# Kernel optimization log

Measured on AMD Instinct MI355X. Metric: run time of the kernel, lower is better.

Reference implementation:

```python
import jax, jax.numpy as jnp
import numpy as np

G, S = 4, 2
EPS_GN, EPS_COS = 1e-5, 1e-8


def group_norm(x, w, b, groups):
    B, C, H, W = x.shape
    xg = x.reshape(B, groups, C // groups, H, W)
    m = xg.mean(axis=(2, 3, 4), keepdims=True)
    v = ((xg - m) ** 2).mean(axis=(2, 3, 4), keepdims=True)
    xn = ((xg - m) / jnp.sqrt(v + EPS_GN)).reshape(B, C, H, W)
    return xn * w[None, :, None, None] + b[None, :, None, None]


def compute_similarity(x, k=3, dilation=2):
    # cosine similarity (over channels) between each pixel and its 8 dilated
    # neighbors (zero padded, unfold row-major order, center dropped)
    B, C, H, W = x.shape
    pad = (k // 2) * dilation
    xp = jnp.pad(x, ((0, 0), (0, 0), (pad, pad), (pad, pad)))
    cn = jnp.sqrt(jnp.sum(x * x, axis=1))  # (B,H,W)
    sims = []
    for ki in range(k):
        for kj in range(k):
            if ki == k // 2 and kj == k // 2:
                continue
            nb = jax.lax.dynamic_slice(xp, (0, 0, ki * dilation, kj * dilation), (B, C, H, W))
            dot = jnp.sum(x * nb, axis=1)
            nn_ = jnp.sqrt(jnp.sum(nb * nb, axis=1))
            sims.append(dot / jnp.maximum(cn * nn_, EPS_COS))
    return jnp.stack(sims, axis=1)  # (B, k*k-1, H, W)


def conv1x1_bn(x, w, sc, bi):
    # 1x1 conv (no bias) followed by eval-mode BN folded to per-channel scale/shift
    return jnp.einsum('oc,bchw->bohw', w, x) * sc[None, :, None, None] + bi[None, :, None, None]


def pixel_unshuffle(x, r):
    B, C, H, W = x.shape
    return x.reshape(B, C, H // r, r, W // r, r).transpose(0, 1, 3, 5, 2, 4).reshape(B, C * r * r, H // r, W // r)


def pixel_shuffle(x, r):
    B, C, H, W = x.shape
    return x.reshape(B, C // (r * r), r, r, H, W).transpose(0, 1, 4, 2, 5, 3).reshape(B, C // (r * r), H * r, W * r)


def init_pos(dtype):
    h = jnp.arange((-S + 1) / 2, (S - 1) / 2 + 1, dtype=dtype) / S  # [-0.25, 0.25]
    t = jnp.stack(jnp.meshgrid(h, h, indexing='ij')).transpose(0, 2, 1)  # (2,2,2)
    return jnp.tile(t, (1, G, 1)).reshape(1, -1, 1, 1)  # (1, 2*g*s*s, 1, 1)


def grid_sample_border(x, grid):
    # bilinear, align_corners=False, padding_mode='border'
    N, C, H, W = x.shape
    gx = jnp.clip(((grid[..., 0] + 1) * W - 1) / 2, 0.0, W - 1.0)
    gy = jnp.clip(((grid[..., 1] + 1) * H - 1) / 2, 0.0, H - 1.0)
    x0 = jnp.floor(gx)
    y0 = jnp.floor(gy)
    wx = (gx - x0)[..., None]
    wy = (gy - y0)[..., None]
    x0i = x0.astype(jnp.int32)
    y0i = y0.astype(jnp.int32)
    x1i = jnp.minimum(x0i + 1, W - 1)
    y1i = jnp.minimum(y0i + 1, H - 1)
    bi = jnp.arange(N)[:, None, None]
    v00 = x[bi, :, y0i, x0i]  # (N,Ho,Wo,C)
    v01 = x[bi, :, y0i, x1i]
    v10 = x[bi, :, y1i, x0i]
    v11 = x[bi, :, y1i, x1i]
    out = (v00 * (1 - wx) + v01 * wx) * (1 - wy) + (v10 * (1 - wx) + v11 * wx) * wy
    return out.transpose(0, 3, 1, 2)  # (N,C,Ho,Wo)


def sample(x, offset):
    b, _, h, w = offset.shape
    off = offset.reshape(b, 2, -1, h, w)  # (b,2,g*s*s,h,w)
    cw = jnp.arange(w, dtype=x.dtype) + 0.5
    ch = jnp.arange(h, dtype=x.dtype) + 0.5
    coords = jnp.stack(jnp.meshgrid(cw, ch, indexing='ij')).transpose(0, 2, 1)[None, :, None]  # (1,2,1,h,w)
    norm = jnp.array([w, h], dtype=x.dtype).reshape(1, 2, 1, 1, 1)
    coords = 2 * (coords + off) / norm - 1
    grid = pixel_shuffle(coords.reshape(b, -1, h, w), S)  # (b, 2*g, s*h, s*w)
    grid = grid.reshape(b, 2, G, S * h, S * w).transpose(0, 2, 3, 4, 1).reshape(b * G, S * h, S * w, 2)
    C = x.shape[1]
    out = grid_sample_border(x.reshape(b * G, C // G, h, w), grid)
    return out.reshape(b, C, S * h, S * w)


def setup_inputs() -> dict:
    key = jax.random.key(0)
    ks = jax.random.split(key, 24)
    B, C, H, W, CF = 2, 64, 128, 128, 256
    CIN, C2L, C2H = C + 8, 2 * G * S * S, 2 * G
    f = jnp.float32
    return {
        'x_l': jax.random.normal(ks[0], (B, C, H, W), f),
        'x_h': jax.random.normal(ks[1], (B, C, 2 * H, 2 * W), f),
        'feat2sample': jax.random.normal(ks[2], (B, CF, H, W), f),
        'gn_l_w': 1.0 + 0.1 * jax.random.normal(ks[3], (C,), f),
        'gn_l_b': 0.1 * jax.random.normal(ks[4], (C,), f),
        'gn_h_w': 1.0 + 0.1 * jax.random.normal(ks[5], (C,), f),
        'gn_h_b': 0.1 * jax.random.normal(ks[6], (C,), f),
        'w_off': 0.02 * jax.random.normal(ks[7], (C2L, CIN), f),
        's_off': 1.0 + 0.05 * jax.random.normal(ks[8], (C2L,), f),
        'b_off': 0.02 * jax.random.normal(ks[9], (C2L,), f),
        'w_off_h': 0.02 * jax.random.normal(ks[10], (C2H, CIN), f),
        's_off_h': 1.0 + 0.05 * jax.random.normal(ks[11], (C2H,), f),
        'b_off_h': 0.02 * jax.random.normal(ks[12], (C2H,), f),
        'w_ds': 0.02 * jax.random.normal(ks[13], (C2L, CIN), f),
        's_ds': 1.0 + 0.05 * jax.random.normal(ks[14], (C2L,), f),
        'b_ds': 0.02 * jax.random.normal(ks[15], (C2L,), f),
        'w_ds_h': 0.02 * jax.random.normal(ks[16], (C2H, CIN), f),
        's_ds_h': 1.0 + 0.05 * jax.random.normal(ks[17], (C2H,), f),
        'b_ds_h': 0.02 * jax.random.normal(ks[18], (C2H,), f),
    }


def reference(x_l, x_h, feat2sample, gn_l_w, gn_l_b, gn_h_w, gn_h_b,
              w_off, s_off, b_off, w_off_h, s_off_h, b_off_h,
              w_ds, s_ds, b_ds, w_ds_h, s_ds_h, b_ds_h):
    xl = group_norm(x_l, gn_l_w, gn_l_b, x_l.shape[1] // 8)
    xh = group_norm(x_h, gn_h_w, gn_h_b, x_h.shape[1] // 8)
    sim_l = jnp.concatenate([xl, compute_similarity(xl)], axis=1)  # (B, C+8, H, W)
    sim_h = jnp.concatenate([xh, compute_similarity(xh)], axis=1)  # (B, C+8, 2H, 2W)
    off = conv1x1_bn(sim_l, w_off, s_off, b_off) \
        + pixel_unshuffle(conv1x1_bn(sim_h, w_off_h, s_off_h, b_off_h), S)
    gate = jax.nn.sigmoid(conv1x1_bn(sim_l, w_ds, s_ds, b_ds)
                          + pixel_unshuffle(conv1x1_bn(sim_h, w_ds_h, s_ds_h, b_ds_h), S))
    offset = off * gate + init_pos(xl.dtype)  # (B, 2*g*s*s, H, W)
    return sample(feat2sample, offset)
```

## Files before the change

### kernel.cpp

```cpp
#include <hip/hip_runtime.h>
#include <math.h>

#define BATCH 2
#define CCH 64
#define HL 128
#define WL 128
#define HH 256
#define WH 256
#define CFCH 256
#define CIN 72

constexpr long WS_AL   = 0;
constexpr long WS_BL   = 128;
constexpr long WS_AH   = 256;
constexpr long WS_BH   = 384;
constexpr long WS_OFFL = 512;
constexpr long WS_DSL  = WS_OFFL + 1048576;
constexpr long WS_OFFH = WS_DSL + 1048576;
constexpr long WS_DSH  = WS_OFFH + 1048576;
constexpr long WS_CRD  = WS_DSH + 1048576;
constexpr long WS_PART = WS_CRD + 1048576;

__global__ void k_stats1(const float* __restrict__ xl, const float* __restrict__ xh,
                         float* __restrict__ ws) {
  int blk = blockIdx.x;
  const float* x;
  long base;
  int gg, slice;
  if (blk < 256) {
    int g = blk >> 4; slice = blk & 15;
    x = xl; gg = g;
    base = (long)g * 8 * (HL * WL) + (long)slice * 8192;
  } else {
    int id = blk - 256;
    int g = id >> 6; slice = id & 63;
    x = xh; gg = 16 + g;
    base = (long)g * 8 * (HH * WH) + (long)slice * 8192;
  }
  const float4* p = (const float4*)(x + base);
  float s = 0.f, s2 = 0.f;
  #pragma unroll
  for (int k = 0; k < 8; k++) {
    float4 v = p[threadIdx.x + k * 256];
    s  += v.x + v.y + v.z + v.w;
    s2 += v.x * v.x + v.y * v.y + v.z * v.z + v.w * v.w;
  }
  __shared__ float sh1[256], sh2[256];
  sh1[threadIdx.x] = s; sh2[threadIdx.x] = s2;
  __syncthreads();
  for (int off = 128; off > 0; off >>= 1) {
    if (threadIdx.x < off) {
      sh1[threadIdx.x] += sh1[threadIdx.x + off];
      sh2[threadIdx.x] += sh2[threadIdx.x + off];
    }
    __syncthreads();
  }
  if (threadIdx.x == 0) {
    ws[WS_PART + (gg * 64 + slice) * 2]     = sh1[0];
    ws[WS_PART + (gg * 64 + slice) * 2 + 1] = sh2[0];
  }
}

__global__ void k_stats2(const float* __restrict__ gwl, const float* __restrict__ gbl,
                         const float* __restrict__ gwh, const float* __restrict__ gbh,
                         float* __restrict__ ws) {
  int blk = blockIdx.x;
  bool high = blk >= 16;
  int id = blk & 15;
  int b = id >> 3, g = id & 7;
  int gg = high ? 16 + id : id;
  int nsl = high ? 64 : 16;
  long n = high ? (long)8 * HH * WH : (long)8 * HL * WL;
  float s = 0.f, s2 = 0.f;
  for (int i = threadIdx.x; i < nsl; i += 64) {
    s  += ws[WS_PART + (gg * 64 + i) * 2];
    s2 += ws[WS_PART + (gg * 64 + i) * 2 + 1];
  }
  for (int off = 32; off > 0; off >>= 1) {
    s  += __shfl_down(s, off);
    s2 += __shfl_down(s2, off);
  }
  __shared__ float shm[2];
  if (threadIdx.x == 0) { shm[0] = s; shm[1] = s2; }
  __syncthreads();
  if (threadIdx.x < 8) {
    float mean = shm[0] / (float)n;
    float var  = shm[1] / (float)n - mean * mean;
    float inv  = rsqrtf(var + 1e-5f);
    int c = g * 8 + threadIdx.x;
    const float* gw = high ? gwh : gwl;
    const float* gb = high ? gbh : gbl;
    float a  = gw[c] * inv;
    float bb = gb[c] - mean * a;
    float* abase = ws + (high ? WS_AH : WS_AL);
    abase[b * CCH + c] = a;
    abase[128 + b * CCH + c] = bb;
  }
}

template<int HSZ, int WSZ, int NOUT>
__global__ __launch_bounds__(512) void k_head(
                       const float* __restrict__ x,
                       const float* __restrict__ w_off, const float* __restrict__ w_ds,
                       const float* __restrict__ s_off, const float* __restrict__ b_off,
                       const float* __restrict__ s_ds,  const float* __restrict__ b_ds,
                       const float* __restrict__ acoef, const float* __restrict__ bcoef,
                       float* __restrict__ out_off, float* __restrict__ out_ds) {
  constexpr int HW   = HSZ * WSZ;
  constexpr int half = NOUT / 2;
  constexpr int PER  = NOUT / 8;
  __shared__ float wsm[NOUT * CIN];
  __shared__ float xc[CCH * 64];
  __shared__ float psum[8 * 64];
  __shared__ float sims[8 * 64];
  __shared__ float asm_[CCH], bsm_[CCH];

  int tid = threadIdx.x;
  int px = tid & 63;
  int t  = tid >> 6;
  int gpix = blockIdx.x * 64 + px;
  int xq = gpix % WSZ;
  int yq = (gpix / WSZ) % HSZ;
  int bq = gpix / (WSZ * HSZ);

  for (int i = tid; i < NOUT * CIN; i += 512) {
    int o = i / CIN, c = i % CIN;
    wsm[i] = (o < half) ? w_off[o * CIN + c] : w_ds[(o - half) * CIN + c];
  }
  if (tid < CCH)            asm_[tid] = acoef[bq * CCH + tid];
  else if (tid < 2 * CCH)   bsm_[tid - CCH] = bcoef[bq * CCH + tid - CCH];
  __syncthreads();

  const float* ptr = x + ((long)(bq * CCH)) * HW + yq * WSZ + xq;

  {
    float ss = 0.f;
    #pragma unroll
    for (int k = 0; k < 8; k++) {
      int c = t * 8 + k;
      float v = fmaf(asm_[c], ptr[(long)c * HW], bsm_[c]);
      xc[c * 64 + px] = v;
      ss += v * v;
    }
    psum[t * 64 + px] = ss;
  }
  __syncthreads();

  {
    const int dyv[8] = {-2,-2,-2, 0, 0, 2, 2, 2};
    const int dxv[8] = {-2, 0, 2,-2, 2,-2, 0, 2};
    int dy = dyv[t], dx = dxv[t];
    int yn = yq + dy;
    int xn = xq + dx;
    bool ok = (yn >= 0 && yn < HSZ && xn >= 0 && xn < WSZ);
    float dot = 0.f, nbq = 0.f;
    if (ok) {
      const float* nptr = ptr + (long)dy * WSZ + dx;
      #pragma unroll 16
      for (int c = 0; c < CCH; c++) {
        float nb = fmaf(asm_[c], nptr[(long)c * HW], bsm_[c]);
        float xv = xc[c * 64 + px];
        dot += xv * nb;
        nbq += nb * nb;
      }
    }
    float cs = 0.f;
    #pragma unroll
    for (int tt = 0; tt < 8; tt++) cs += psum[tt * 64 + px];
    float cnc = sqrtf(cs);
    sims[t * 64 + px] = dot / fmaxf(cnc * sqrtf(nbq), 1e-8f);
  }
  __syncthreads();

  {
    float sv[8];
    #pragma unroll
    for (int j = 0; j < 8; j++) sv[j] = sims[j * 64 + px];
    float acc[PER];
    #pragma unroll
    for (int ol = 0; ol < PER; ol++) acc[ol] = 0.f;
    int o0 = t * PER;
    #pragma unroll 4
    for (int c = 0; c < CCH; c += 4) {
      float x0v = xc[(c + 0) * 64 + px];
      float x1v = xc[(c + 1) * 64 + px];
      float x2v = xc[(c + 2) * 64 + px];
      float x3v = xc[(c + 3) * 64 + px];
      #pragma unroll
      for (int ol = 0; ol < PER; ol++) {
        const float4 w4 = *(const float4*)&wsm[(o0 + ol) * CIN + c];
        acc[ol] += w4.x * x0v + w4.y * x1v + w4.z * x2v + w4.w * x3v;
      }
    }
    #pragma unroll
    for (int ol = 0; ol < PER; ol++) {
      const float4 wa = *(const float4*)&wsm[(o0 + ol) * CIN + 64];
      const float4 wb = *(const float4*)&wsm[(o0 + ol) * CIN + 68];
      acc[ol] += wa.x * sv[0] + wa.y * sv[1] + wa.z * sv[2] + wa.w * sv[3]
               + wb.x * sv[4] + wb.y * sv[5] + wb.z * sv[6] + wb.w * sv[7];
    }
    #pragma unroll
    for (int ol = 0; ol < PER; ol++) {
      int o = o0 + ol;
      float v;
      float* dst;
      int oo;
      if (o < half) { v = acc[ol] * s_off[o] + b_off[o];             dst = out_off; oo = o; }
      else          { v = acc[ol] * s_ds[o - half] + b_ds[o - half]; dst = out_ds;  oo = o - half; }
      dst[((long)(bq * half + oo)) * HW + yq * WSZ + xq] = v;
    }
  }
}

__global__ __launch_bounds__(256) void k_combine(float* __restrict__ ws) {
  int idx = blockIdx.x * blockDim.x + threadIdx.x;
  int x = idx & 127;
  int y = (idx >> 7) & 127;
  int sub = (idx >> 14) & 15;
  int b = idx >> 18;
  int sdx = sub & 1, sdy = (sub >> 1) & 1;

  const float* offl = ws + WS_OFFL;
  const float* dsl  = ws + WS_DSL;
  const float* offh = ws + WS_OFFH;
  const float* dsh  = ws + WS_DSH;

  int lidx = idx + b * (16 * HL * WL);
  float ol0 = offl[lidx],               dl0 = dsl[lidx];
  float ol1 = offl[lidx + 16 * HL * WL], dl1 = dsl[lidx + 16 * HL * WL];
  int Y = 2 * y + sdy, X = 2 * x + sdx;
  long h0 = ((long)(b * 8 + (sub >> 2)) * HH + Y) * WH + X;
  long h1 = h0 + (long)4 * HH * WH;
  float oh0 = offh[h0], dh0 = dsh[h0];
  float oh1 = offh[h1], dh1 = dsh[h1];
  float gate0 = 1.f / (1.f + expf(-(dl0 + dh0)));
  float gate1 = 1.f / (1.f + expf(-(dl1 + dh1)));
  float offx = (ol0 + oh0) * gate0 + (sdx ? 0.25f : -0.25f);
  float offy = (ol1 + oh1) * gate1 + (sdy ? 0.25f : -0.25f);
  float gx = fminf(fmaxf((float)x + offx, 0.f), (float)(WL - 1));
  float gy = fminf(fmaxf((float)y + offy, 0.f), (float)(HL - 1));
  float2* crd = (float2*)(ws + WS_CRD);
  crd[idx] = float2{gx, gy};
}

__global__ __launch_bounds__(512, 6) void k_sample(const float* __restrict__ feat,
                                                   const float* __restrict__ ws,
                                                   float* __restrict__ out) {
  __shared__ float sbuf[8 * 512];
  int bid = (blockIdx.x & 7) * 128 + (blockIdx.x >> 3);
  int y = bid & 127;
  int g = (bid >> 7) & 3;
  int b = bid >> 9;
  int w = threadIdx.x >> 6;
  int l = threadIdx.x & 63;

  const float2* crd = (const float2*)(ws + WS_CRD);
  int   pack[8];
  float wxa[8], wya[8];
  bool fb = false;
  #pragma unroll
  for (int Yp = 0; Yp < 2; Yp++) {
    #pragma unroll
    for (int j = 0; j < 4; j++) {
      int xx = 2 * l + (j >> 1);
      int sub = 4 * g + 2 * Yp + (j & 1);
      float2 cc = crd[((long)(b * 16 + sub)) * (HL * WL) + y * WL + xx];
      float gx = cc.x, gy = cc.y;
      float fx0 = floorf(gx), fy0 = floorf(gy);
      int x0 = (int)fx0, y0 = (int)fy0;
      float wx = gx - fx0, wy = gy - fy0;
      if (x0 >= WL - 1) { x0 = WL - 2; wx = 1.f; }
      if (y0 >= HL - 1) { y0 = HL - 2; wy = 1.f; }
      fb = fb || (y0 < y - 1) || (y0 > y + 1);
      pack[Yp * 4 + j] = y0 * WL + x0;
      wxa[Yp * 4 + j] = wx;
      wya[Yp * 4 + j] = wy;
    }
  }
  int ladj = w * 512 + (1 - y) * 128;

  int row0 = l >> 5;
  int row1 = 2 + row0;
  int fr0 = min(max(y - 1 + row0, 0), HL - 1);
  int fr1 = min(max(y - 1 + row1, 0), HL - 1);
  int x4 = (l & 31) * 4;
  long cbase = (long)(b * CFCH + g * 64 + w);
  const float* ps0 = feat + (cbase * HL + fr0) * WL + x4;
  const float* ps1 = feat + (cbase * HL + fr1) * WL + x4;
  const float* pg  = feat + cbase * (HL * WL);
  int s0 = w * 512 + row0 * 128 + x4;
  int s1 = w * 512 + row1 * 128 + x4;
  float* po0 = out + (cbase * HH + 2 * y) * WH + 4 * l;
  float* po1 = po0 + WH;
  const long CSTEP  = (long)8 * HL * WL;
  const long OSTEP  = (long)8 * HH * WH;

  float4 t0 = *(const float4*)ps0;
  float4 t1 = *(const float4*)ps1;
  #pragma unroll 1
  for (int k = 0; k < 8; k++) {
    *(float4*)&sbuf[s0] = t0;
    *(float4*)&sbuf[s1] = t1;
    if (k < 7) {
      ps0 += CSTEP; ps1 += CSTEP;
      t0 = *(const float4*)ps0;
      t1 = *(const float4*)ps1;
    }
    float v[2][4];
    if (!fb) {
      #pragma unroll
      for (int Yp = 0; Yp < 2; Yp++) {
        #pragma unroll
        for (int j = 0; j < 4; j++) {
          int li = pack[Yp * 4 + j] + ladj;
          float wx = wxa[Yp * 4 + j], wy = wya[Yp * 4 + j];
          float s00 = sbuf[li], s01 = sbuf[li + 1];
          float s10 = sbuf[li + 128], s11 = sbuf[li + 129];
          v[Yp][j] = (s00 * (1.f - wx) + s01 * wx) * (1.f - wy)
                   + (s10 * (1.f - wx) + s11 * wx) * wy;
        }
      }
    } else {
      #pragma unroll
      for (int Yp = 0; Yp < 2; Yp++) {
        #pragma unroll
        for (int j = 0; j < 4; j++) {
          const float* pp = pg + pack[Yp * 4 + j];
          float wx = wxa[Yp * 4 + j], wy = wya[Yp * 4 + j];
          float s00 = pp[0], s01 = pp[1];
          float s10 = pp[WL], s11 = pp[WL + 1];
          v[Yp][j] = (s00 * (1.f - wx) + s01 * wx) * (1.f - wy)
                   + (s10 * (1.f - wx) + s11 * wx) * wy;
        }
      }
    }
    *(float4*)po0 = make_float4(v[0][0], v[0][1], v[0][2], v[0][3]);
    *(float4*)po1 = make_float4(v[1][0], v[1][1], v[1][2], v[1][3]);
    po0 += OSTEP; po1 += OSTEP;
    pg  += CSTEP;
  }
}

extern "C" void kernel_launch(void* const* d_in, const int* in_sizes, int n_in,
                              void* d_out, int out_size, void* d_ws, size_t ws_size,
                              hipStream_t stream) {
  const float* x_l     = (const float*)d_in[0];
  const float* x_h     = (const float*)d_in[1];
  const float* feat    = (const float*)d_in[2];
  const float* gn_l_w  = (const float*)d_in[3];
  const float* gn_l_b  = (const float*)d_in[4];
  const float* gn_h_w  = (const float*)d_in[5];
  const float* gn_h_b  = (const float*)d_in[6];
  const float* w_off   = (const float*)d_in[7];
  const float* s_off   = (const float*)d_in[8];
  const float* b_off   = (const float*)d_in[9];
  const float* w_off_h = (const float*)d_in[10];
  const float* s_off_h = (const float*)d_in[11];
  const float* b_off_h = (const float*)d_in[12];
  const float* w_ds    = (const float*)d_in[13];
  const float* s_ds    = (const float*)d_in[14];
  const float* b_ds    = (const float*)d_in[15];
  const float* w_ds_h  = (const float*)d_in[16];
  const float* s_ds_h  = (const float*)d_in[17];
  const float* b_ds_h  = (const float*)d_in[18];
  float* ws  = (float*)d_ws;
  float* out = (float*)d_out;

  k_stats1<<<1280, 256, 0, stream>>>(x_l, x_h, ws);
  k_stats2<<<32, 64, 0, stream>>>(gn_l_w, gn_l_b, gn_h_w, gn_h_b, ws);
  k_head<HL, WL, 64><<<(BATCH * HL * WL) / 64, 512, 0, stream>>>(
      x_l, w_off, w_ds, s_off, b_off, s_ds, b_ds,
      ws + WS_AL, ws + WS_BL, ws + WS_OFFL, ws + WS_DSL);
  k_head<HH, WH, 16><<<(BATCH * HH * WH) / 64, 512, 0, stream>>>(
      x_h, w_off_h, w_ds_h, s_off_h, b_off_h, s_ds_h, b_ds_h,
      ws + WS_AH, ws + WS_BH, ws + WS_OFFH, ws + WS_DSH);
  k_combine<<<(BATCH * 16 * HL * WL) / 256, 256, 0, stream>>>(ws);
  k_sample<<<BATCH * 4 * HL, 512, 0, stream>>>(feat, ws, out);
}
```

Measured before the change: 99.25 us.

## Split sampling blocks to one output row each, doubling grid size

```diff
diff --git a/kernel.cpp b/kernel.cpp
--- a/kernel.cpp
+++ b/kernel.cpp
@@ -243,39 +243,38 @@
   crd[idx] = float2{gx, gy};
 }
 
-__global__ __launch_bounds__(512, 6) void k_sample(const float* __restrict__ feat,
+__global__ __launch_bounds__(512, 8) void k_sample(const float* __restrict__ feat,
                                                    const float* __restrict__ ws,
                                                    float* __restrict__ out) {
   __shared__ float sbuf[8 * 512];
-  int bid = (blockIdx.x & 7) * 128 + (blockIdx.x >> 3);
-  int y = bid & 127;
-  int g = (bid >> 7) & 3;
-  int b = bid >> 9;
+  int bid = (blockIdx.x & 7) * 256 + (blockIdx.x >> 3);
+  int Y = bid & 255;
+  int g = (bid >> 8) & 3;
+  int b = bid >> 10;
+  int y = Y >> 1, sdy = Y & 1;
   int w = threadIdx.x >> 6;
   int l = threadIdx.x & 63;
 
   const float2* crd = (const float2*)(ws + WS_CRD);
-  int   pack[8];
-  float wxa[8], wya[8];
+  int   pack[4];
+  float wxa[4], wya[4];
   bool fb = false;
   #pragma unroll
-  for (int Yp = 0; Yp < 2; Yp++) {
-    #pragma unroll
-    for (int j = 0; j < 4; j++) {
-      int xx = 2 * l + (j >> 1);
-      int sub = 4 * g + 2 * Yp + (j & 1);
-      float2 cc = crd[((long)(b * 16 + sub)) * (HL * WL) + y * WL + xx];
-      float gx = cc.x, gy = cc.y;
-      float fx0 = floorf(gx), fy0 = floorf(gy);
-      int x0 = (int)fx0, y0 = (int)fy0;
-      float wx = gx - fx0, wy = gy - fy0;
-      if (x0 >= WL - 1) { x0 = WL - 2; wx = 1.f; }
-      if (y0 >= HL - 1) { y0 = HL - 2; wy = 1.f; }
-      fb = fb || (y0 < y - 1) || (y0 > y + 1);
-      pack[Yp * 4 + j] = y0 * WL + x0;
-      wxa[Yp * 4 + j] = wx;
-      wya[Yp * 4 + j] = wy;
-    }
+  for (int j = 0; j < 4; j++) {
+    int X = 4 * l + j;
+    int x = X >> 1, sdx = X & 1;
+    int sub = 4 * g + 2 * sdy + sdx;
+    float2 cc = crd[((long)(b * 16 + sub)) * (HL * WL) + y * WL + x];
+    float gx = cc.x, gy = cc.y;
+    float fx0 = floorf(gx), fy0 = floorf(gy);
+    int x0 = (int)fx0, y0 = (int)fy0;
+    float wx = gx - fx0, wy = gy - fy0;
+    if (x0 >= WL - 1) { x0 = WL - 2; wx = 1.f; }
+    if (y0 >= HL - 1) { y0 = HL - 2; wy = 1.f; }
+    fb = fb || (y0 < y - 1) || (y0 > y + 1);
+    pack[j] = y0 * WL + x0;
+    wxa[j] = wx;
+    wya[j] = wy;
   }
   int ladj = w * 512 + (1 - y) * 128;
 
@@ -290,8 +289,7 @@
   const float* pg  = feat + cbase * (HL * WL);
   int s0 = w * 512 + row0 * 128 + x4;
   int s1 = w * 512 + row1 * 128 + x4;
-  float* po0 = out + (cbase * HH + 2 * y) * WH + 4 * l;
-  float* po1 = po0 + WH;
+  float* po = out + (cbase * HH + Y) * WH + 4 * l;
   const long CSTEP  = (long)8 * HL * WL;
   const long OSTEP  = (long)8 * HH * WH;
 
@@ -306,38 +304,31 @@
       t0 = *(const float4*)ps0;
       t1 = *(const float4*)ps1;
     }
-    float v[2][4];
+    float v[4];
     if (!fb) {
       #pragma unroll
-      for (int Yp = 0; Yp < 2; Yp++) {
-        #pragma unroll
-        for (int j = 0; j < 4; j++) {
-          int li = pack[Yp * 4 + j] + ladj;
-          float wx = wxa[Yp * 4 + j], wy = wya[Yp * 4 + j];
-          float s00 = sbuf[li], s01 = sbuf[li + 1];
-          float s10 = sbuf[li + 128], s11 = sbuf[li + 129];
-          v[Yp][j] = (s00 * (1.f - wx) + s01 * wx) * (1.f - wy)
-                   + (s10 * (1.f - wx) + s11 * wx) * wy;
-        }
+      for (int j = 0; j < 4; j++) {
+        int li = pack[j] + ladj;
+        float wx = wxa[j], wy = wya[j];
+        float s00 = sbuf[li], s01 = sbuf[li + 1];
+        float s10 = sbuf[li + 128], s11 = sbuf[li + 129];
+        v[j] = (s00 * (1.f - wx) + s01 * wx) * (1.f - wy)
+             + (s10 * (1.f - wx) + s11 * wx) * wy;
       }
     } else {
       #pragma unroll
-      for (int Yp = 0; Yp < 2; Yp++) {
-        #pragma unroll
-        for (int j = 0; j < 4; j++) {
-          const float* pp = pg + pack[Yp * 4 + j];
-          float wx = wxa[Yp * 4 + j], wy = wya[Yp * 4 + j];
-          float s00 = pp[0], s01 = pp[1];
-          float s10 = pp[WL], s11 = pp[WL + 1];
-          v[Yp][j] = (s00 * (1.f - wx) + s01 * wx) * (1.f - wy)
-                   + (s10 * (1.f - wx) + s11 * wx) * wy;
-        }
+      for (int j = 0; j < 4; j++) {
+        const float* pp = pg + pack[j];
+        float wx = wxa[j], wy = wya[j];
+        float s00 = pp[0], s01 = pp[1];
+        float s10 = pp[WL], s11 = pp[WL + 1];
+        v[j] = (s00 * (1.f - wx) + s01 * wx) * (1.f - wy)
+             + (s10 * (1.f - wx) + s11 * wx) * wy;
       }
     }
-    *(float4*)po0 = make_float4(v[0][0], v[0][1], v[0][2], v[0][3]);
-    *(float4*)po1 = make_float4(v[1][0], v[1][1], v[1][2], v[1][3]);
-    po0 += OSTEP; po1 += OSTEP;
-    pg  += CSTEP;
+    *(float4*)po = make_float4(v[0], v[1], v[2], v[3]);
+    po += OSTEP;
+    pg += CSTEP;
   }
 }
 
@@ -375,5 +366,5 @@
       x_h, w_off_h, w_ds_h, s_off_h, b_off_h, s_ds_h, b_ds_h,
       ws + WS_AH, ws + WS_BH, ws + WS_OFFH, ws + WS_DSH);
   k_combine<<<(BATCH * 16 * HL * WL) / 256, 256, 0, stream>>>(ws);
-  k_sample<<<BATCH * 4 * HL, 512, 0, stream>>>(feat, ws, out);
-}
+  k_sample<<<BATCH * 4 * HH, 512, 0, stream>>>(feat, ws, out);
+}
```

Result: no change. 97.98 us (-1.3%).
